# Optimization experiments

Hardware: AMD Instinct MI355X
Metric: run time of the kernel (lower is better)

The kernel has to match this reference:

```python
import math
import jax, jax.numpy as jnp
import numpy as np

SAMPLE_RATE = 16000
N_BANDS = 3
_F_DARK = jnp.array([270.0, 800.0, 2300.0], dtype=jnp.float32)
_F_NEUTRAL = jnp.array([500.0, 1500.0, 2500.0], dtype=jnp.float32)
_F_BRIGHT = jnp.array([730.0, 2100.0, 3000.0], dtype=jnp.float32)
_Q_DARK = jnp.array([5.0, 5.0, 5.0], dtype=jnp.float32)
_Q_NEUTRAL = jnp.array([8.0, 8.0, 8.0], dtype=jnp.float32)
_Q_BRIGHT = jnp.array([12.0, 12.0, 12.0], dtype=jnp.float32)


def _interpolate_formants(level):
    # level: [B] in [0,1] -> freqs, qs: [B, n_bands]
    t_low = jnp.clip(level * 2.0, 0.0, 1.0)[:, None]
    t_high = jnp.clip((level - 0.5) * 2.0, 0.0, 1.0)[:, None]
    use_high = (level >= 0.5)[:, None]
    freqs_lo = (1.0 - t_low) * _F_DARK + t_low * _F_NEUTRAL
    qs_lo = (1.0 - t_low) * _Q_DARK + t_low * _Q_NEUTRAL
    freqs_hi = (1.0 - t_high) * _F_NEUTRAL + t_high * _F_BRIGHT
    qs_hi = (1.0 - t_high) * _Q_NEUTRAL + t_high * _Q_BRIGHT
    freqs = jnp.where(use_high, freqs_hi, freqs_lo)
    qs = jnp.where(use_high, qs_hi, qs_lo)
    return freqs, qs


def _biquad_bandpass_coeffs(freq_hz, q):
    # freq_hz, q: [B, n_bands] -> coeffs each [B, n_bands]; b1 is 0
    omega = (2.0 * math.pi / SAMPLE_RATE) * freq_hz
    sin_o = jnp.sin(omega)
    cos_o = jnp.cos(omega)
    alpha = sin_o / (2.0 * jnp.maximum(q, 0.5))
    a0 = 1.0 + alpha
    b0 = alpha / a0
    b2 = -alpha / a0
    a1 = (-2.0 * cos_o) / a0
    a2 = (1.0 - alpha) / a0
    return b0, b2, a1, a2


def setup_inputs() -> dict:
    key = jax.random.key(0)
    k1, k2 = jax.random.split(key)
    B, S = 256, 131072
    audio = jax.random.normal(k1, (B, S), dtype=jnp.float32)
    resonance_level = jax.random.uniform(k2, (B,), dtype=jnp.float32)
    return {"audio": audio, "resonance_level": resonance_level}


def reference(audio, resonance_level):
    B, S = audio.shape
    level = jnp.clip(resonance_level.astype(audio.dtype), 0.0, 1.0)
    freqs, qs = _interpolate_formants(level)          # [B, nb]
    b0, b2, a1, a2 = _biquad_bandpass_coeffs(freqs, qs)
    # broadcast coeffs to [nb, B] for the scan
    b0, b2, a1, a2 = (c.T for c in (b0, b2, a1, a2))
    nb = N_BANDS
    zeros = jnp.zeros((nb, B), dtype=audio.dtype)
    inv_sqrt_nb = 1.0 / math.sqrt(nb)

    def step(carry, x_t):
        # carry: (x1, x2, y1, y2) each [nb, B]; x_t: [B]
        x1, x2, y1, y2 = carry
        y = b0 * x_t[None, :] + b2 * x2 - a1 * y1 - a2 * y2  # [nb, B]
        new_x1 = jnp.broadcast_to(x_t[None, :], (nb, B))
        return (new_x1, x1, y, y1), jnp.sum(y, axis=0) * inv_sqrt_nb

    _, out = jax.lax.scan(step, (zeros, zeros, zeros, zeros), audio.T)  # out: [S, B]
    return out.T
```

## Files before the change

kernel.cpp:

```cpp
#include <hip/hip_runtime.h>
#include <math.h>

#ifndef M_PI
#define M_PI 3.14159265358979323846
#endif

#define BATCHES 256
#define S_LEN   131072

#define TPB   320
#define MAINT 256
#define CCH   16
#define SEGS  32
#define SEG_SAMPS (MAINT * CCH)
#define WCH   48
#define OBSTR 20
#define SCAN_STR 305
#define H_OFF 5120
#define LDSF  (H_OFF + 3 * CCH)

typedef float v4f __attribute__((ext_vector_type(4)));

__device__ __forceinline__ void compute_coeffs(float level_in, float b0[3], float na1[3], float na2[3]) {
    const float FD[3] = {270.0f, 800.0f, 2300.0f};
    const float FN[3] = {500.0f, 1500.0f, 2500.0f};
    const float FB[3] = {730.0f, 2100.0f, 3000.0f};
    float level = fminf(fmaxf(level_in, 0.0f), 1.0f);
    float t_low  = fminf(fmaxf(level * 2.0f, 0.0f), 1.0f);
    float t_high = fminf(fmaxf((level - 0.5f) * 2.0f, 0.0f), 1.0f);
    bool hi = (level >= 0.5f);
    const float W0 = (float)(2.0 * M_PI / 16000.0);
    #pragma unroll
    for (int k = 0; k < 3; ++k) {
        float f, q;
        if (hi) { f = (1.0f - t_high) * FN[k] + t_high * FB[k];
                  q = (1.0f - t_high) * 8.0f  + t_high * 12.0f; }
        else    { f = (1.0f - t_low) * FD[k] + t_low * FN[k];
                  q = (1.0f - t_low) * 5.0f  + t_low * 8.0f; }
        float omega = W0 * f;
        float sn = __sinf(omega), cs = __cosf(omega);
        float alpha = sn / (2.0f * fmaxf(q, 0.5f));
        float a0 = 1.0f + alpha;
        b0[k]  = alpha / a0;
        na1[k] = (2.0f * cs) / a0;
        na2[k] = -((1.0f - alpha) / a0);
    }
}

#define STEP3(XT, XTM2, SUMV)                                                    \
    {                                                                            \
        float d = (XT) - (XTM2);                                                 \
        float e0 = fmaf(b0[0], d, na2[0] * y2[0]);                               \
        float e1 = fmaf(b0[1], d, na2[1] * y2[1]);                               \
        float e2 = fmaf(b0[2], d, na2[2] * y2[2]);                               \
        float yy0 = fmaf(na1[0], y1[0], e0);                                     \
        float yy1 = fmaf(na1[1], y1[1], e1);                                     \
        float yy2 = fmaf(na1[2], y1[2], e2);                                     \
        y2[0] = y1[0]; y1[0] = yy0;                                              \
        y2[1] = y1[1]; y1[1] = yy1;                                              \
        y2[2] = y1[2]; y1[2] = yy2;                                              \
        SUMV = (yy0 + yy1 + yy2);                                                \
    }

#define MMUL(R00,R01,R10,R11, X00,X01,X10,X11, Y00,Y01,Y10,Y11)                  \
    {                                                                            \
        R00 = X00*Y00 + X01*Y10; R01 = X00*Y01 + X01*Y11;                        \
        R10 = X10*Y00 + X11*Y10; R11 = X10*Y01 + X11*Y11;                        \
    }

__global__ __launch_bounds__(TPB, 2)
void formant_onepass(const float* __restrict__ x, const float* __restrict__ lvl,
                     float* __restrict__ out)
{
    __shared__ float lds[LDSF];

    const int tid = threadIdx.x;
    const int row = blockIdx.x >> 5;
    const int seg = blockIdx.x & (SEGS - 1);

    float b0[3], na1[3], na2[3];
    compute_coeffs(lvl[row], b0, na1, na2);

    const float* xrow = x + (size_t)row * S_LEN;
    const size_t segBase = (size_t)seg * SEG_SAMPS;

    float4 szs[4];

    if (tid < MAINT) {
        const float* xc = xrow + segBase + (size_t)tid * CCH;
        float xm1 = 0.f, xm2 = 0.f;
        if (seg > 0 || tid > 0) { float2 t2 = *(const float2*)(xc - 2); xm2 = t2.x; xm1 = t2.y; }
        float y1[3] = {0.f,0.f,0.f}, y2[3] = {0.f,0.f,0.f};
        const float4* xv = (const float4*)xc;
        float4 buf[4];
        #pragma unroll
        for (int j = 0; j < 4; ++j) buf[j] = xv[j];
        #pragma unroll
        for (int i = 0; i < 4; ++i) {
            float4 q = buf[i];
            float4 o;
            STEP3(q.x, xm2, o.x)
            STEP3(q.y, xm1, o.y)
            STEP3(q.z, q.x, o.z)
            STEP3(q.w, q.y, o.w)
            xm2 = q.z; xm1 = q.w;
            szs[i] = o;
        }
        lds[0*SCAN_STR + WCH + tid] = y1[0];
        lds[1*SCAN_STR + WCH + tid] = y2[0];
        lds[2*SCAN_STR + WCH + tid] = y1[1];
        lds[3*SCAN_STR + WCH + tid] = y2[1];
        lds[4*SCAN_STR + WCH + tid] = y1[2];
        lds[5*SCAN_STR + WCH + tid] = y2[2];
    }
    else if (tid < MAINT + WCH) {
        const int wid = tid - MAINT;
        if (seg == 0) {
            #pragma unroll
            for (int e = 0; e < 6; ++e) lds[e*SCAN_STR + wid] = 0.f;
        } else {
            const float* xw = xrow + segBase - (size_t)(WCH * CCH) + (size_t)wid * CCH;
            float2 t2 = *(const float2*)(xw - 2);
            float y1[3] = {0.f,0.f,0.f}, y2[3] = {0.f,0.f,0.f};
            float p2 = t2.x, p1 = t2.y, dummy;
            const float4* xv = (const float4*)xw;
            float4 buf[4];
            #pragma unroll
            for (int j = 0; j < 4; ++j) buf[j] = xv[j];
            #pragma unroll
            for (int i = 0; i < 4; ++i) {
                float4 q = buf[i];
                STEP3(q.x, p2, dummy)
                STEP3(q.y, p1, dummy)
                STEP3(q.z, q.x, dummy)
                STEP3(q.w, q.y, dummy)
                p2 = q.z; p1 = q.w;
            }
            (void)dummy;
            lds[0*SCAN_STR + wid] = y1[0];
            lds[1*SCAN_STR + wid] = y2[0];
            lds[2*SCAN_STR + wid] = y1[1];
            lds[3*SCAN_STR + wid] = y2[1];
            lds[4*SCAN_STR + wid] = y1[2];
            lds[5*SCAN_STR + wid] = y2[2];
        }
    }
    __syncthreads();

    {
        const int wv = tid >> 6, ln = tid & 63;
        if (wv < 3) {
            const float A1 = na1[wv], A2 = na2[wv];
            float hm1 = 1.f, hm2 = 0.f, hm3 = 0.f;
            for (int i = 0; i < CCH; ++i) {
                float h = fmaf(A1, hm1, A2 * hm2);
                hm3 = hm2; hm2 = hm1; hm1 = h;
                if (ln == 0) lds[H_OFF + wv * CCH + i] = h;
            }
            const float H00 = hm1, H01 = A2 * hm2;
            const float H10 = hm2, H11 = A2 * hm3;

            float* z1p = lds + (2*wv) * SCAN_STR;
            float* z2p = lds + (2*wv + 1) * SCAN_STR;

            const int cnt = (ln < 48) ? 5 : 4;
            const int beg = (ln < 48) ? 5 * ln : 240 + 4 * (ln - 48);

            float s1 = 0.f, s2 = 0.f;
            for (int j = 0; j < cnt; ++j) {
                float z1 = z1p[beg + j], z2 = z2p[beg + j];
                float n1 = z1 + H00 * s1 + H01 * s2;
                float n2 = z2 + H10 * s1 + H11 * s2;
                s1 = n1; s2 = n2;
            }
            float B00,B01,B10,B11, C00,C01,C10,C11;
            MMUL(B00,B01,B10,B11, H00,H01,H10,H11, H00,H01,H10,H11)
            MMUL(C00,C01,C10,C11, B00,B01,B10,B11, B00,B01,B10,B11)
            float A00 = C00, A01 = C01, A10 = C10, A11 = C11;
            if (cnt == 5) {
                float D00,D01,D10,D11;
                MMUL(D00,D01,D10,D11, C00,C01,C10,C11, H00,H01,H10,H11)
                A00 = D00; A01 = D01; A10 = D10; A11 = D11;
            }
            float bb1 = s1, bb2 = s2;
            for (int d = 1; d < 64; d <<= 1) {
                float iA00 = __shfl_up(A00, d), iA01 = __shfl_up(A01, d);
                float iA10 = __shfl_up(A10, d), iA11 = __shfl_up(A11, d);
                float ib1  = __shfl_up(bb1, d), ib2  = __shfl_up(bb2, d);
                if (ln >= d) {
                    float nb1 = A00 * ib1 + A01 * ib2 + bb1;
                    float nb2 = A10 * ib1 + A11 * ib2 + bb2;
                    float n00, n01, n10, n11;
                    MMUL(n00,n01,n10,n11, A00,A01,A10,A11, iA00,iA01,iA10,iA11)
                    A00 = n00; A01 = n01; A10 = n10; A11 = n11;
                    bb1 = nb1; bb2 = nb2;
                }
            }
            float e1 = __shfl_up(bb1, 1), e2 = __shfl_up(bb2, 1);
            if (ln == 0) { e1 = 0.f; e2 = 0.f; }

            s1 = e1; s2 = e2;
            for (int j = 0; j < cnt; ++j) {
                int w = beg + j;
                float z1 = z1p[w], z2 = z2p[w];
                z1p[w] = s1; z2p[w] = s2;
                float n1 = z1 + H00 * s1 + H01 * s2;
                float n2 = z2 + H10 * s1 + H11 * s2;
                s1 = n1; s2 = n2;
            }
        }
    }
    __syncthreads();

    float c1k[3], c2k[3];
    if (tid < MAINT) {
        #pragma unroll
        for (int k = 0; k < 3; ++k) {
            c1k[k] = lds[(2*k) * SCAN_STR + WCH + tid];
            c2k[k] = na2[k] * lds[(2*k + 1) * SCAN_STR + WCH + tid];
        }
    }
    __syncthreads();

    if (tid < MAINT) {
        const float is3 = 0.57735026918962576f;
        float* myst = lds + tid * OBSTR;
        float hp[3] = {1.f, 1.f, 1.f};
        #pragma unroll
        for (int i = 0; i < 4; ++i) {
            float4 s = szs[i];
            float o0 = s.x, o1 = s.y, o2 = s.z, o3 = s.w;
            #pragma unroll
            for (int k = 0; k < 3; ++k) {
                const float4 hv = *(const float4*)&lds[H_OFF + k * CCH + 4 * i];
                o0 = fmaf(c1k[k], hv.x, fmaf(c2k[k], hp[k], o0));
                o1 = fmaf(c1k[k], hv.y, fmaf(c2k[k], hv.x,  o1));
                o2 = fmaf(c1k[k], hv.z, fmaf(c2k[k], hv.y,  o2));
                o3 = fmaf(c1k[k], hv.w, fmaf(c2k[k], hv.z,  o3));
                hp[k] = hv.w;
            }
            v4f o = { o0 * is3, o1 * is3, o2 * is3, o3 * is3 };
            *(v4f*)(myst + 4 * i) = o;
        }
    }
    __syncthreads();

    {
        float* obase = out + (size_t)row * S_LEN + segBase;
        #pragma unroll
        for (int j = 0; j < 3; ++j) {
            const int f = j * TPB + tid;
            const v4f o = *(const v4f*)(lds + (f >> 2) * OBSTR + (f & 3) * 4);
            __builtin_nontemporal_store(o, (v4f*)(obase + (size_t)f * 4));
        }
        if (tid < 1024 - 3 * TPB) {
            const int f = 3 * TPB + tid;
            const v4f o = *(const v4f*)(lds + (f >> 2) * OBSTR + (f & 3) * 4);
            __builtin_nontemporal_store(o, (v4f*)(obase + (size_t)f * 4));
        }
    }
}

extern "C" void kernel_launch(void* const* d_in, const int* in_sizes, int n_in,
                              void* d_out, int out_size, void* d_ws, size_t ws_size,
                              hipStream_t stream) {
    const float* audio = (const float*)d_in[0];
    const float* level = (const float*)d_in[1];
    float* out = (float*)d_out;
    (void)in_sizes; (void)n_in; (void)d_ws; (void)ws_size; (void)out_size;

    formant_onepass<<<BATCHES * SEGS, TPB, 0, stream>>>(audio, level, out);
}
```

Measured before the change: 57.53 us.

## Process two adjacent segments per block, chaining state to skip second warm-up

```diff
diff --git a/kernel.cpp b/kernel.cpp
--- a/kernel.cpp
+++ b/kernel.cpp
@@ -13,11 +13,18 @@
 #define CCH   16
 #define SEGS  32
 #define SEG_SAMPS (MAINT * CCH)
+#define PAIRS (SEGS / 2)
 #define WCH   48
-#define OBSTR 20
-#define SCAN_STR 305
-#define H_OFF 5120
-#define LDSF  (H_OFF + 3 * CCH)
+
+#define OBSTR   20
+#define STG_OFF 0
+#define SC1_OFF 5120
+#define SC1_STR 305
+#define SC2_OFF 6950
+#define SC2_STR 257
+#define H_OFF   8492
+#define E0_OFF  8540
+#define LDSF    8548
 
 typedef float v4f __attribute__((ext_vector_type(4)));
 
@@ -69,27 +76,28 @@
     }
 
 __global__ __launch_bounds__(TPB, 2)
-void formant_onepass(const float* __restrict__ x, const float* __restrict__ lvl,
-                     float* __restrict__ out)
+void formant_pair(const float* __restrict__ x, const float* __restrict__ lvl,
+                  float* __restrict__ out)
 {
     __shared__ float lds[LDSF];
 
-    const int tid = threadIdx.x;
-    const int row = blockIdx.x >> 5;
-    const int seg = blockIdx.x & (SEGS - 1);
+    const int tid  = threadIdx.x;
+    const int row  = blockIdx.x >> 4;
+    const int pair = blockIdx.x & (PAIRS - 1);
 
     float b0[3], na1[3], na2[3];
     compute_coeffs(lvl[row], b0, na1, na2);
 
     const float* xrow = x + (size_t)row * S_LEN;
-    const size_t segBase = (size_t)seg * SEG_SAMPS;
-
-    float4 szs[4];
+    const size_t baseA = (size_t)(2 * pair) * SEG_SAMPS;
+    const size_t baseB = baseA + SEG_SAMPS;
+
+    float4 szsA[4];
 
     if (tid < MAINT) {
-        const float* xc = xrow + segBase + (size_t)tid * CCH;
+        const float* xc = xrow + baseA + (size_t)tid * CCH;
         float xm1 = 0.f, xm2 = 0.f;
-        if (seg > 0 || tid > 0) { float2 t2 = *(const float2*)(xc - 2); xm2 = t2.x; xm1 = t2.y; }
+        if (pair > 0 || tid > 0) { float2 t2 = *(const float2*)(xc - 2); xm2 = t2.x; xm1 = t2.y; }
         float y1[3] = {0.f,0.f,0.f}, y2[3] = {0.f,0.f,0.f};
         const float4* xv = (const float4*)xc;
         float4 buf[4];
@@ -104,22 +112,21 @@
             STEP3(q.z, q.x, o.z)
             STEP3(q.w, q.y, o.w)
             xm2 = q.z; xm1 = q.w;
-            szs[i] = o;
-        }
-        lds[0*SCAN_STR + WCH + tid] = y1[0];
-        lds[1*SCAN_STR + WCH + tid] = y2[0];
-        lds[2*SCAN_STR + WCH + tid] = y1[1];
-        lds[3*SCAN_STR + WCH + tid] = y2[1];
-        lds[4*SCAN_STR + WCH + tid] = y1[2];
-        lds[5*SCAN_STR + WCH + tid] = y2[2];
-    }
-    else if (tid < MAINT + WCH) {
+            szsA[i] = o;
+        }
+        lds[SC1_OFF + 0*SC1_STR + WCH + tid] = y1[0];
+        lds[SC1_OFF + 1*SC1_STR + WCH + tid] = y2[0];
+        lds[SC1_OFF + 2*SC1_STR + WCH + tid] = y1[1];
+        lds[SC1_OFF + 3*SC1_STR + WCH + tid] = y2[1];
+        lds[SC1_OFF + 4*SC1_STR + WCH + tid] = y1[2];
+        lds[SC1_OFF + 5*SC1_STR + WCH + tid] = y2[2];
+    } else if (tid < MAINT + WCH) {
         const int wid = tid - MAINT;
-        if (seg == 0) {
-            #pragma unroll
-            for (int e = 0; e < 6; ++e) lds[e*SCAN_STR + wid] = 0.f;
+        if (pair == 0) {
+            #pragma unroll
+            for (int e = 0; e < 6; ++e) lds[SC1_OFF + e*SC1_STR + wid] = 0.f;
         } else {
-            const float* xw = xrow + segBase - (size_t)(WCH * CCH) + (size_t)wid * CCH;
+            const float* xw = xrow + baseA - (size_t)(WCH * CCH) + (size_t)wid * CCH;
             float2 t2 = *(const float2*)(xw - 2);
             float y1[3] = {0.f,0.f,0.f}, y2[3] = {0.f,0.f,0.f};
             float p2 = t2.x, p1 = t2.y, dummy;
@@ -137,15 +144,25 @@
                 p2 = q.z; p1 = q.w;
             }
             (void)dummy;
-            lds[0*SCAN_STR + wid] = y1[0];
-            lds[1*SCAN_STR + wid] = y2[0];
-            lds[2*SCAN_STR + wid] = y1[1];
-            lds[3*SCAN_STR + wid] = y2[1];
-            lds[4*SCAN_STR + wid] = y1[2];
-            lds[5*SCAN_STR + wid] = y2[2];
+            lds[SC1_OFF + 0*SC1_STR + wid] = y1[0];
+            lds[SC1_OFF + 1*SC1_STR + wid] = y2[0];
+            lds[SC1_OFF + 2*SC1_STR + wid] = y1[1];
+            lds[SC1_OFF + 3*SC1_STR + wid] = y2[1];
+            lds[SC1_OFF + 4*SC1_STR + wid] = y1[2];
+            lds[SC1_OFF + 5*SC1_STR + wid] = y2[2];
         }
     }
     __syncthreads();
+
+    float4 bufB[4];
+    float xmB1 = 0.f, xmB2 = 0.f;
+    if (tid < MAINT) {
+        const float* xcB = xrow + baseB + (size_t)tid * CCH;
+        const float4* xvB = (const float4*)xcB;
+        #pragma unroll
+        for (int j = 0; j < 4; ++j) bufB[j] = xvB[j];
+        float2 t2 = *(const float2*)(xcB - 2); xmB2 = t2.x; xmB1 = t2.y;
+    }
 
     {
         const int wv = tid >> 6, ln = tid & 63;
@@ -160,8 +177,8 @@
             const float H00 = hm1, H01 = A2 * hm2;
             const float H10 = hm2, H11 = A2 * hm3;
 
-            float* z1p = lds + (2*wv) * SCAN_STR;
-            float* z2p = lds + (2*wv + 1) * SCAN_STR;
+            float* z1p = lds + SC1_OFF + (2*wv) * SC1_STR;
+            float* z2p = lds + SC1_OFF + (2*wv + 1) * SC1_STR;
 
             const int cnt = (ln < 48) ? 5 : 4;
             const int beg = (ln < 48) ? 5 * ln : 240 + 4 * (ln - 48);
@@ -208,35 +225,162 @@
                 float n2 = z2 + H10 * s1 + H11 * s2;
                 s1 = n1; s2 = n2;
             }
+            if (ln == 63) { lds[E0_OFF + 2*wv] = s1; lds[E0_OFF + 2*wv + 1] = s2; }
         }
     }
     __syncthreads();
 
-    float c1k[3], c2k[3];
+    float4 szsB[4];
     if (tid < MAINT) {
+        float c1A[3], c2A[3];
         #pragma unroll
         for (int k = 0; k < 3; ++k) {
-            c1k[k] = lds[(2*k) * SCAN_STR + WCH + tid];
-            c2k[k] = na2[k] * lds[(2*k + 1) * SCAN_STR + WCH + tid];
+            c1A[k] = lds[SC1_OFF + (2*k) * SC1_STR + WCH + tid];
+            c2A[k] = na2[k] * lds[SC1_OFF + (2*k + 1) * SC1_STR + WCH + tid];
+        }
+        {
+            float y1[3] = {0.f,0.f,0.f}, y2[3] = {0.f,0.f,0.f};
+            float p2 = xmB2, p1 = xmB1;
+            #pragma unroll
+            for (int i = 0; i < 4; ++i) {
+                float4 q = bufB[i];
+                float4 o;
+                STEP3(q.x, p2, o.x)
+                STEP3(q.y, p1, o.y)
+                STEP3(q.z, q.x, o.z)
+                STEP3(q.w, q.y, o.w)
+                p2 = q.z; p1 = q.w;
+                szsB[i] = o;
+            }
+            lds[SC2_OFF + 0*SC2_STR + tid] = y1[0];
+            lds[SC2_OFF + 1*SC2_STR + tid] = y2[0];
+            lds[SC2_OFF + 2*SC2_STR + tid] = y1[1];
+            lds[SC2_OFF + 3*SC2_STR + tid] = y2[1];
+            lds[SC2_OFF + 4*SC2_STR + tid] = y1[2];
+            lds[SC2_OFF + 5*SC2_STR + tid] = y2[2];
+        }
+        {
+            const float is3 = 0.57735026918962576f;
+            float* myst = lds + STG_OFF + tid * OBSTR;
+            float hp[3] = {1.f, 1.f, 1.f};
+            #pragma unroll
+            for (int i = 0; i < 4; ++i) {
+                float4 s = szsA[i];
+                float o0 = s.x, o1 = s.y, o2 = s.z, o3 = s.w;
+                #pragma unroll
+                for (int k = 0; k < 3; ++k) {
+                    const float4 hv = *(const float4*)&lds[H_OFF + k * CCH + 4 * i];
+                    o0 = fmaf(c1A[k], hv.x, fmaf(c2A[k], hp[k], o0));
+                    o1 = fmaf(c1A[k], hv.y, fmaf(c2A[k], hv.x,  o1));
+                    o2 = fmaf(c1A[k], hv.z, fmaf(c2A[k], hv.y,  o2));
+                    o3 = fmaf(c1A[k], hv.w, fmaf(c2A[k], hv.z,  o3));
+                    hp[k] = hv.w;
+                }
+                v4f o = { o0 * is3, o1 * is3, o2 * is3, o3 * is3 };
+                *(v4f*)(myst + 4 * i) = o;
+            }
         }
     }
     __syncthreads();
 
+    {
+        float* obase = out + (size_t)row * S_LEN + baseA;
+        #pragma unroll
+        for (int j = 0; j < 3; ++j) {
+            const int f = j * TPB + tid;
+            const v4f o = *(const v4f*)(lds + STG_OFF + (f >> 2) * OBSTR + (f & 3) * 4);
+            __builtin_nontemporal_store(o, (v4f*)(obase + (size_t)f * 4));
+        }
+        if (tid < 1024 - 3 * TPB) {
+            const int f = 3 * TPB + tid;
+            const v4f o = *(const v4f*)(lds + STG_OFF + (f >> 2) * OBSTR + (f & 3) * 4);
+            __builtin_nontemporal_store(o, (v4f*)(obase + (size_t)f * 4));
+        }
+    }
+
+    {
+        const int wv = tid >> 6, ln = tid & 63;
+        if (wv < 3) {
+            const float A1 = na1[wv], A2 = na2[wv];
+            float hm1 = 1.f, hm2 = 0.f, hm3 = 0.f;
+            for (int i = 0; i < CCH; ++i) {
+                float h = fmaf(A1, hm1, A2 * hm2);
+                hm3 = hm2; hm2 = hm1; hm1 = h;
+            }
+            const float H00 = hm1, H01 = A2 * hm2;
+            const float H10 = hm2, H11 = A2 * hm3;
+
+            float* z1p = lds + SC2_OFF + (2*wv) * SC2_STR;
+            float* z2p = lds + SC2_OFF + (2*wv + 1) * SC2_STR;
+
+            const float e01 = lds[E0_OFF + 2*wv], e02 = lds[E0_OFF + 2*wv + 1];
+            const int beg = 4 * ln;
+
+            float s1 = (ln == 0) ? e01 : 0.f;
+            float s2 = (ln == 0) ? e02 : 0.f;
+            #pragma unroll
+            for (int j = 0; j < 4; ++j) {
+                float z1 = z1p[beg + j], z2 = z2p[beg + j];
+                float n1 = z1 + H00 * s1 + H01 * s2;
+                float n2 = z2 + H10 * s1 + H11 * s2;
+                s1 = n1; s2 = n2;
+            }
+            float B00,B01,B10,B11;
+            MMUL(B00,B01,B10,B11, H00,H01,H10,H11, H00,H01,H10,H11)
+            float A00,A01,A10,A11;
+            MMUL(A00,A01,A10,A11, B00,B01,B10,B11, B00,B01,B10,B11)
+            float bb1 = s1, bb2 = s2;
+            for (int d = 1; d < 64; d <<= 1) {
+                float iA00 = __shfl_up(A00, d), iA01 = __shfl_up(A01, d);
+                float iA10 = __shfl_up(A10, d), iA11 = __shfl_up(A11, d);
+                float ib1  = __shfl_up(bb1, d), ib2  = __shfl_up(bb2, d);
+                if (ln >= d) {
+                    float nb1 = A00 * ib1 + A01 * ib2 + bb1;
+                    float nb2 = A10 * ib1 + A11 * ib2 + bb2;
+                    float n00, n01, n10, n11;
+                    MMUL(n00,n01,n10,n11, A00,A01,A10,A11, iA00,iA01,iA10,iA11)
+                    A00 = n00; A01 = n01; A10 = n10; A11 = n11;
+                    bb1 = nb1; bb2 = nb2;
+                }
+            }
+            float e1 = __shfl_up(bb1, 1), e2 = __shfl_up(bb2, 1);
+            if (ln == 0) { e1 = e01; e2 = e02; }
+
+            s1 = e1; s2 = e2;
+            #pragma unroll
+            for (int j = 0; j < 4; ++j) {
+                int w = beg + j;
+                float z1 = z1p[w], z2 = z2p[w];
+                z1p[w] = s1; z2p[w] = s2;
+                float n1 = z1 + H00 * s1 + H01 * s2;
+                float n2 = z2 + H10 * s1 + H11 * s2;
+                s1 = n1; s2 = n2;
+            }
+        }
+    }
+    __syncthreads();
+
     if (tid < MAINT) {
+        float c1B[3], c2B[3];
+        #pragma unroll
+        for (int k = 0; k < 3; ++k) {
+            c1B[k] = lds[SC2_OFF + (2*k) * SC2_STR + tid];
+            c2B[k] = na2[k] * lds[SC2_OFF + (2*k + 1) * SC2_STR + tid];
+        }
         const float is3 = 0.57735026918962576f;
-        float* myst = lds + tid * OBSTR;
+        float* myst = lds + STG_OFF + tid * OBSTR;
         float hp[3] = {1.f, 1.f, 1.f};
         #pragma unroll
         for (int i = 0; i < 4; ++i) {
-            float4 s = szs[i];
+            float4 s = szsB[i];
             float o0 = s.x, o1 = s.y, o2 = s.z, o3 = s.w;
             #pragma unroll
             for (int k = 0; k < 3; ++k) {
                 const float4 hv = *(const float4*)&lds[H_OFF + k * CCH + 4 * i];
-                o0 = fmaf(c1k[k], hv.x, fmaf(c2k[k], hp[k], o0));
-                o1 = fmaf(c1k[k], hv.y, fmaf(c2k[k], hv.x,  o1));
-                o2 = fmaf(c1k[k], hv.z, fmaf(c2k[k], hv.y,  o2));
-                o3 = fmaf(c1k[k], hv.w, fmaf(c2k[k], hv.z,  o3));
+                o0 = fmaf(c1B[k], hv.x, fmaf(c2B[k], hp[k], o0));
+                o1 = fmaf(c1B[k], hv.y, fmaf(c2B[k], hv.x,  o1));
+                o2 = fmaf(c1B[k], hv.z, fmaf(c2B[k], hv.y,  o2));
+                o3 = fmaf(c1B[k], hv.w, fmaf(c2B[k], hv.z,  o3));
                 hp[k] = hv.w;
             }
             v4f o = { o0 * is3, o1 * is3, o2 * is3, o3 * is3 };
@@ -246,16 +390,16 @@
     __syncthreads();
 
     {
-        float* obase = out + (size_t)row * S_LEN + segBase;
+        float* obase = out + (size_t)row * S_LEN + baseB;
         #pragma unroll
         for (int j = 0; j < 3; ++j) {
             const int f = j * TPB + tid;
-            const v4f o = *(const v4f*)(lds + (f >> 2) * OBSTR + (f & 3) * 4);
+            const v4f o = *(const v4f*)(lds + STG_OFF + (f >> 2) * OBSTR + (f & 3) * 4);
             __builtin_nontemporal_store(o, (v4f*)(obase + (size_t)f * 4));
         }
         if (tid < 1024 - 3 * TPB) {
             const int f = 3 * TPB + tid;
-            const v4f o = *(const v4f*)(lds + (f >> 2) * OBSTR + (f & 3) * 4);
+            const v4f o = *(const v4f*)(lds + STG_OFF + (f >> 2) * OBSTR + (f & 3) * 4);
             __builtin_nontemporal_store(o, (v4f*)(obase + (size_t)f * 4));
         }
     }
@@ -269,5 +413,5 @@
     float* out = (float*)d_out;
     (void)in_sizes; (void)n_in; (void)d_ws; (void)ws_size; (void)out_size;
 
-    formant_onepass<<<BATCHES * SEGS, TPB, 0, stream>>>(audio, level, out);
+    formant_pair<<<BATCHES * PAIRS, TPB, 0, stream>>>(audio, level, out);
 }
```

Result: slower. 60.63 us (+5.4%).
